# Kernel tuning notes

Hardware: AMD Instinct MI355X
Metric: run time of the kernel (lower is better)

Reference implementation:

```python
import jax, jax.numpy as jnp
import numpy as np

B, S, E, H = 2, 2048, 768, 8
D = E // H  # 96
SCALING = D ** (-0.5)


def setup_inputs() -> dict:
    key = jax.random.key(0)
    ks = jax.random.split(key, 7)
    sd = E ** -0.5
    return {
        "x": jax.random.normal(ks[0], (B, S, E), jnp.float32),
        "Wq": jax.random.normal(ks[1], (E, E), jnp.float32) * sd,
        "bq": jax.random.normal(ks[2], (E,), jnp.float32) * 0.02,
        "Wk": jax.random.normal(ks[3], (E, E), jnp.float32) * sd,
        "bk": jax.random.normal(ks[4], (E,), jnp.float32) * 0.02,
        "Wo": jax.random.normal(ks[5], (E, E), jnp.float32) * sd,
        "bo": jax.random.normal(ks[6], (E,), jnp.float32) * 0.02,
    }


def _split_heads(t):
    # [B, S, E] -> [B, H, S, D]
    return t.reshape(B, S, H, D).transpose(0, 2, 1, 3)


def reference(x, Wq, bq, Wk, bk, Wo, bo):
    q = _split_heads(x @ Wq + bq)
    k = _split_heads(x @ Wk + bk)
    # NOTE: faithful to source bug — values use the KEY projection
    v = _split_heads(x @ Wk + bk)
    energies = jnp.einsum("bhqd,bhkd->bhqk", q, k)  # [B,H,S,S]
    # NOTE: faithful to source — scaling applied AFTER softmax
    attn = jax.nn.softmax(energies, axis=-1) * SCALING
    out = jnp.einsum("bhqk,bhkd->bhqd", attn, v)
    out = out.transpose(0, 2, 1, 3).reshape(B, S, E)
    return out @ Wo + bo
```

## Files before the change

kernel.cpp:

```cpp
#include <hip/hip_runtime.h>
#include <hip/hip_bf16.h>
#include <math.h>
#include <stdint.h>

#define B_DIM 2
#define S_DIM 2048
#define E_DIM 768
#define H_DIM 8
#define D_DIM 96
#define M_DIM (B_DIM*S_DIM)
#define SCALE_F 0.10206207261596575f

typedef _Float16 f16x8 __attribute__((ext_vector_type(8)));
typedef float    f32x4  __attribute__((ext_vector_type(4)));
typedef float    f32x16 __attribute__((ext_vector_type(16)));

#define MFMA16H(a,b,c) __builtin_amdgcn_mfma_f32_16x16x32_f16(a,b,c,0,0,0)
#define MFMA32H(a,b,c) __builtin_amdgcn_mfma_f32_32x32x16_f16(a,b,c,0,0,0)

__device__ inline unsigned short f2h(float f) {
    return __builtin_bit_cast(unsigned short, (_Float16)f);
}

__device__ inline void gload16(const void* g, void* l) {
    auto gp = reinterpret_cast<const __attribute__((address_space(1))) uint32_t*>(
        reinterpret_cast<uintptr_t>(g));
    auto lp = reinterpret_cast<__attribute__((address_space(3))) uint32_t*>(
        reinterpret_cast<uintptr_t>(l));
    __builtin_amdgcn_global_load_lds(gp, lp, 16, 0, 0);
}

__global__ __launch_bounds__(256) void prep_kernel(
    const float* __restrict__ X,
    const float* __restrict__ W0, const float* __restrict__ W1,
    const float* __restrict__ W2,
    unsigned short* __restrict__ Xf,
    unsigned short* __restrict__ T0, unsigned short* __restrict__ T1,
    unsigned short* __restrict__ T2)
{
    const int tid = threadIdx.x;
    if (blockIdx.x < 3072) {
        int i = (blockIdx.x * 256 + tid) * 4;
        float4 v = *(const float4*)(X + i);
        ushort4 h;
        h.x = f2h(v.x); h.y = f2h(v.y); h.z = f2h(v.z); h.w = f2h(v.w);
        *(ushort4*)(Xf + i) = h;
        return;
    }
    int idx = blockIdx.x - 3072;
    int z = idx / 144, rem = idx % 144;
    const float* W; unsigned short* T;
    if (z == 0)      { W = W0; T = T0; }
    else if (z == 1) { W = W1; T = T1; }
    else             { W = W2; T = T2; }
    int k0 = (rem / 12) << 6, n0 = (rem % 12) << 6;

    __shared__ float tile[64][65];
    const int r = tid >> 4, c4 = (tid & 15) << 2;
    #pragma unroll
    for (int i = 0; i < 4; ++i) {
        float4 v = *(const float4*)(W + (size_t)(k0 + r + i*16)*E_DIM + n0 + c4);
        tile[r + i*16][c4+0] = v.x; tile[r + i*16][c4+1] = v.y;
        tile[r + i*16][c4+2] = v.z; tile[r + i*16][c4+3] = v.w;
    }
    __syncthreads();
    #pragma unroll
    for (int i = 0; i < 4; ++i) {
        int n = r + i*16;
        ushort4 h;
        h.x = f2h(tile[c4+0][n]); h.y = f2h(tile[c4+1][n]);
        h.z = f2h(tile[c4+2][n]); h.w = f2h(tile[c4+3][n]);
        *(ushort4*)(T + (size_t)(n0 + n)*E_DIM + k0 + c4) = h;
    }
}

__global__ __launch_bounds__(256) void gemm_qk_kernel(
    const unsigned short* __restrict__ A, const unsigned short* __restrict__ Bt,
    const float* __restrict__ bq, const float* __restrict__ bk,
    unsigned short* __restrict__ Qf, unsigned short* __restrict__ Kf)
{
    __shared__ unsigned short sA[128*32];
    __shared__ unsigned short sB[64*32];

    const int tid  = threadIdx.x;
    const int lane = tid & 63;
    const int w    = tid >> 6;
    const int qn   = lane & 15, quad = lane >> 4;
    const int wm   = w & 1, wn = w >> 1;
    const int row0 = blockIdx.y << 7;
    const int col0 = blockIdx.x << 6;

    const int sr = tid >> 2;
    const int sk = (tid & 3) << 3;

    const unsigned short* gA = A  + (size_t)(row0 + sr)*E_DIM + sk;
    const unsigned short* gB = Bt + (size_t)(col0 + sr)*E_DIM + sk;

    f32x4 acc[4][2];
    #pragma unroll
    for (int mt = 0; mt < 4; ++mt)
        #pragma unroll
        for (int nt = 0; nt < 2; ++nt)
            { acc[mt][nt][0]=0.f; acc[mt][nt][1]=0.f; acc[mt][nt][2]=0.f; acc[mt][nt][3]=0.f; }

    for (int k0 = 0; k0 < E_DIM; k0 += 32) {
        __syncthreads();
        gload16(gA + k0,            sA + tid*8);
        gload16(gA + 64*E_DIM + k0, sA + 2048 + tid*8);
        gload16(gB + k0,            sB + tid*8);
        __syncthreads();

        f16x8 af[4], bf[2];
        #pragma unroll
        for (int mt = 0; mt < 4; ++mt)
            af[mt] = *(const f16x8*)&sA[(wm*64 + mt*16 + qn)*32 + quad*8];
        #pragma unroll
        for (int nt = 0; nt < 2; ++nt)
            bf[nt] = *(const f16x8*)&sB[(wn*32 + nt*16 + qn)*32 + quad*8];
        #pragma unroll
        for (int mt = 0; mt < 4; ++mt)
            #pragma unroll
            for (int nt = 0; nt < 2; ++nt)
                acc[mt][nt] = MFMA16H(af[mt], bf[nt], acc[mt][nt]);
    }

    #pragma unroll
    for (int nt = 0; nt < 2; ++nt) {
        int n = col0 + wn*32 + nt*16 + qn;
        bool isQ = n < E_DIM;
        float bias = isQ ? bq[n] : bk[n - E_DIM];
        unsigned short* op = isQ ? Qf : Kf;
        int nc = isQ ? n : n - E_DIM;
        #pragma unroll
        for (int mt = 0; mt < 4; ++mt)
            #pragma unroll
            for (int r = 0; r < 4; ++r) {
                int m = row0 + wm*64 + mt*16 + quad*4 + r;
                op[(size_t)m*E_DIM + nc] = f2h(acc[mt][nt][r] + bias);
            }
    }
}

__global__ __launch_bounds__(256) void attn_mfma_kernel(
    const unsigned short* __restrict__ Qf, const unsigned short* __restrict__ Kf,
    unsigned short* __restrict__ O0, unsigned short* __restrict__ O1,
    float2* __restrict__ ml)
{
    __shared__ unsigned short sKh[64][104];
    __shared__ unsigned short sKt[96][72];
    __shared__ unsigned short sPs[128][72];

    const int tid  = threadIdx.x;
    const int w    = tid >> 6;
    const int lane = tid & 63;
    const int col  = lane & 31;
    const int half = lane >> 5;
    const int b    = blockIdx.z >> 1;
    const int kh   = blockIdx.z & 1;
    const int h    = blockIdx.y;
    const int q0   = blockIdx.x << 7;
    const int key0 = kh << 10;

    f16x8 qf[6];
    {
        const size_t ro = ((size_t)(b*S_DIM + q0 + w*32 + col))*E_DIM
                          + h*D_DIM + half*8;
        #pragma unroll
        for (int kc = 0; kc < 6; ++kc)
            qf[kc] = *(const f16x8*)(Qf + ro + kc*16);
    }

    f32x16 o[3];
    #pragma unroll
    for (int nt = 0; nt < 3; ++nt)
        #pragma unroll
        for (int r = 0; r < 16; ++r) o[nt][r] = 0.f;
    float m_i = -INFINITY, l_i = 0.f;

    const bool stager = tid < 128;
    const int st = tid & 127;
    const int sp = st >> 2;
    const int dq = st & 3;

    uint4 r0[3], r1[3];
    if (stager) {
        const size_t g0 = ((size_t)(b*S_DIM + key0 + 2*sp))*E_DIM + h*D_DIM + dq*24;
        #pragma unroll
        for (int i = 0; i < 3; ++i) {
            r0[i] = *(const uint4*)(Kf + g0 + 8*i);
            r1[i] = *(const uint4*)(Kf + g0 + E_DIM + 8*i);
        }
    }

    for (int kt = 0; kt < 16; ++kt) {
        __syncthreads();
        if (stager) {
            #pragma unroll
            for (int i = 0; i < 3; ++i) {
                *(uint4*)&sKh[2*sp  ][dq*24 + 8*i] = r0[i];
                *(uint4*)&sKh[2*sp+1][dq*24 + 8*i] = r1[i];
            }
            const unsigned short* p0 = (const unsigned short*)r0;
            const unsigned short* p1 = (const unsigned short*)r1;
            #pragma unroll
            for (int c = 0; c < 24; ++c) {
                unsigned int pk = (unsigned int)p0[c] | ((unsigned int)p1[c] << 16);
                *(unsigned int*)&sKt[dq*24 + c][2*sp] = pk;
            }
        }
        __syncthreads();

        if (stager && kt + 1 < 16) {
            const size_t g0 = ((size_t)(b*S_DIM + key0 + (kt+1)*64 + 2*sp))*E_DIM
                              + h*D_DIM + dq*24;
            #pragma unroll
            for (int i = 0; i < 3; ++i) {
                r0[i] = *(const uint4*)(Kf + g0 + 8*i);
                r1[i] = *(const uint4*)(Kf + g0 + E_DIM + 8*i);
            }
        }

        f32x16 s[2];
        #pragma unroll
        for (int mt = 0; mt < 2; ++mt) {
            f32x16 acc;
            #pragma unroll
            for (int r = 0; r < 16; ++r) acc[r] = 0.f;
            #pragma unroll
            for (int kc = 0; kc < 6; ++kc) {
                f16x8 ah = *(const f16x8*)&sKh[mt*32 + col][kc*16 + half*8];
                acc = MFMA32H(ah, qf[kc], acc);
            }
            s[mt] = acc;
        }

        float mx = s[0][0];
        #pragma unroll
        for (int mt = 0; mt < 2; ++mt)
            #pragma unroll
            for (int r = 0; r < 16; ++r) mx = fmaxf(mx, s[mt][r]);
        mx = fmaxf(mx, __shfl_xor(mx, 32));

        float m_new = fmaxf(m_i, mx);
        float alpha = __expf(m_i - m_new);
        m_i = m_new;

        float psum = 0.f;
        #pragma unroll
        for (int mt = 0; mt < 2; ++mt)
            #pragma unroll
            for (int g = 0; g < 4; ++g) {
                float e0 = __expf(s[mt][4*g+0] - m_new);
                float e1 = __expf(s[mt][4*g+1] - m_new);
                float e2 = __expf(s[mt][4*g+2] - m_new);
                float e3 = __expf(s[mt][4*g+3] - m_new);
                psum += e0 + e1 + e2 + e3;
                ushort4 pk;
                pk.x = f2h(e0); pk.y = f2h(e1); pk.z = f2h(e2); pk.w = f2h(e3);
                *(ushort4*)&sPs[w*32 + col][mt*32 + 8*g + 4*half] = pk;
            }
        psum += __shfl_xor(psum, 32);
        l_i = l_i * alpha + psum;

        #pragma unroll
        for (int nt = 0; nt < 3; ++nt)
            #pragma unroll
            for (int r = 0; r < 16; ++r) o[nt][r] *= alpha;

        #pragma unroll
        for (int kc = 0; kc < 4; ++kc) {
            f16x8 pb = *(const f16x8*)&sPs[w*32 + col][kc*16 + half*8];
            #pragma unroll
            for (int nt = 0; nt < 3; ++nt) {
                f16x8 va = *(const f16x8*)&sKt[nt*32 + col][kc*16 + half*8];
                o[nt] = MFMA32H(va, pb, o[nt]);
            }
        }
    }

    unsigned short* Ob = (kh ? O1 : O0)
        + ((size_t)(b*S_DIM + q0 + w*32 + col))*E_DIM + h*D_DIM;
    #pragma unroll
    for (int nt = 0; nt < 3; ++nt)
        #pragma unroll
        for (int rg = 0; rg < 4; ++rg) {
            ushort4 pk;
            pk.x = f2h(o[nt][4*rg+0]); pk.y = f2h(o[nt][4*rg+1]);
            pk.z = f2h(o[nt][4*rg+2]); pk.w = f2h(o[nt][4*rg+3]);
            *(ushort4*)(Ob + nt*32 + 8*rg + 4*half) = pk;
        }
    if (lane < 32) {
        int q = q0 + w*32 + lane;
        ml[((size_t)(kh*B_DIM + b)*H_DIM + h)*S_DIM + q] = make_float2(m_i, l_i);
    }
}

__device__ inline float2 mkscale(const float2* __restrict__ ml, int m, int h) {
    int b = m >> 11, q = m & (S_DIM - 1);
    float2 e0 = ml[((size_t)b*H_DIM + h)*S_DIM + q];
    float2 e1 = ml[((size_t)(B_DIM + b)*H_DIM + h)*S_DIM + q];
    float mm = fmaxf(e0.x, e1.x);
    float w0 = __expf(e0.x - mm), w1 = __expf(e1.x - mm);
    float inv = SCALE_F / (e0.y*w0 + e1.y*w1);
    return make_float2(w0*inv, w1*inv);
}

__global__ __launch_bounds__(256) void gemm_out_kernel(
    const unsigned short* __restrict__ O0, const unsigned short* __restrict__ O1,
    const float2* __restrict__ ml, const unsigned short* __restrict__ Bt,
    const float* __restrict__ bo, float* __restrict__ out)
{
    __shared__ unsigned short sA[64*32];
    __shared__ unsigned short sB[64*32];

    const int tid  = threadIdx.x;
    const int lane = tid & 63;
    const int w    = tid >> 6;
    const int qn   = lane & 15, quad = lane >> 4;
    const int wm   = w & 1, wn = w >> 1;
    const int row0 = blockIdx.y << 6;
    const int col0 = blockIdx.x << 6;

    const int ar = tid >> 2;
    const int ak = (tid & 3) << 3;

    const size_t r0o = (size_t)(row0 + ar)*E_DIM;
    const unsigned short* gB = Bt + (size_t)(col0 + ar)*E_DIM + ak;

    f32x4 acc[2][2];
    #pragma unroll
    for (int mt = 0; mt < 2; ++mt)
        #pragma unroll
        for (int nt = 0; nt < 2; ++nt)
            { acc[mt][nt][0]=0.f; acc[mt][nt][1]=0.f; acc[mt][nt][2]=0.f; acc[mt][nt][3]=0.f; }

    f16x8 u0 = *(const f16x8*)(O0 + r0o + ak);
    f16x8 v0 = *(const f16x8*)(O1 + r0o + ak);
    float2 s0 = mkscale(ml, row0 + ar, 0);

    for (int k0 = 0; k0 < E_DIM; k0 += 32) {
        __syncthreads();
        {
            f16x8 c0 = u0 * (_Float16)s0.x + v0 * (_Float16)s0.y;
            *(f16x8*)&sA[ar*32 + ak] = c0;
        }
        gload16(gB + k0, sB + tid*8);
        __syncthreads();

        if (k0 + 32 < E_DIM) {
            int kn = k0 + 32;
            u0 = *(const f16x8*)(O0 + r0o + kn + ak);
            v0 = *(const f16x8*)(O1 + r0o + kn + ak);
            s0 = mkscale(ml, row0 + ar, kn / D_DIM);
        }

        f16x8 af[2], bf[2];
        #pragma unroll
        for (int mt = 0; mt < 2; ++mt)
            af[mt] = *(const f16x8*)&sA[(wm*32 + mt*16 + qn)*32 + quad*8];
        #pragma unroll
        for (int nt = 0; nt < 2; ++nt)
            bf[nt] = *(const f16x8*)&sB[(wn*32 + nt*16 + qn)*32 + quad*8];
        #pragma unroll
        for (int mt = 0; mt < 2; ++mt)
            #pragma unroll
            for (int nt = 0; nt < 2; ++nt)
                acc[mt][nt] = MFMA16H(af[mt], bf[nt], acc[mt][nt]);
    }

    #pragma unroll
    for (int nt = 0; nt < 2; ++nt) {
        int n = col0 + wn*32 + nt*16 + qn;
        float bias = bo[n];
        #pragma unroll
        for (int mt = 0; mt < 2; ++mt)
            #pragma unroll
            for (int r = 0; r < 4; ++r) {
                int m = row0 + wm*32 + mt*16 + quad*4 + r;
                out[(size_t)m*E_DIM + n] = acc[mt][nt][r] + bias;
            }
    }
}

extern "C" void kernel_launch(void* const* d_in, const int* in_sizes, int n_in,
                              void* d_out, int out_size, void* d_ws, size_t ws_size,
                              hipStream_t stream)
{
    const float* x  = (const float*)d_in[0];
    const float* Wq = (const float*)d_in[1];
    const float* bq = (const float*)d_in[2];
    const float* Wk = (const float*)d_in[3];
    const float* bk = (const float*)d_in[4];
    const float* Wo = (const float*)d_in[5];
    const float* bo = (const float*)d_in[6];
    float* out = (float*)d_out;

    const size_t NE = (size_t)M_DIM * E_DIM;
    const size_t WE = (size_t)E_DIM * E_DIM;
    unsigned short* xf    = (unsigned short*)d_ws;
    unsigned short* WqkT  = xf + NE;
    unsigned short* WoT   = WqkT + 2*WE;
    unsigned short* Qf    = WoT + WE;
    unsigned short* Kf    = Qf + NE;
    unsigned short* Oh1   = Kf + NE;
    float2*         mlbuf = (float2*)(Oh1 + NE);
    unsigned short* Oh0   = xf;

    dim3 blk(256);
    hipLaunchKernelGGL(prep_kernel, dim3(3504), blk, 0, stream,
                       x, Wq, Wk, Wo, xf, WqkT, WqkT + WE, WoT);

    hipLaunchKernelGGL(gemm_qk_kernel, dim3(24,32), blk, 0, stream,
                       xf, WqkT, bq, bk, Qf, Kf);

    hipLaunchKernelGGL(attn_mfma_kernel, dim3(S_DIM/128, H_DIM, B_DIM*2), blk, 0,
                       stream, Qf, Kf, Oh0, Oh1, mlbuf);

    hipLaunchKernelGGL(gemm_out_kernel, dim3(12,64), blk, 0, stream,
                       Oh0, Oh1, mlbuf, WoT, bo, out);
}
```

Baseline: 168.6 us.

## Compute softmax row sums via MFMA with ones, widen QK GEMM k-step

The attention kernel drops the scalar row-sum reduction and cross-lane shuffle. It instead computes the softmax denominator with an extra MFMA that multiplies a ones vector by the P tile, so the sum is accumulated on the matrix cores and rescaled by alpha through one element. The row max uses three-input max trees, and fp16 packing uses the packed round-toward-zero convert. The QK projection GEMM loads 64-wide K chunks per sync, halving the number of barriers, at the cost of doubled LDS use; the extra MFMA per kc step adds matrix work and accumulator registers.

```diff
diff --git a/kernel.cpp b/kernel.cpp
--- a/kernel.cpp
+++ b/kernel.cpp
@@ -11,6 +11,7 @@
 #define M_DIM (B_DIM*S_DIM)
 #define SCALE_F 0.10206207261596575f
 
+typedef _Float16 f16x2 __attribute__((ext_vector_type(2)));
 typedef _Float16 f16x8 __attribute__((ext_vector_type(8)));
 typedef float    f32x4  __attribute__((ext_vector_type(4)));
 typedef float    f32x16 __attribute__((ext_vector_type(16)));
@@ -20,6 +21,12 @@
 
 __device__ inline unsigned short f2h(float f) {
     return __builtin_bit_cast(unsigned short, (_Float16)f);
+}
+__device__ inline unsigned int pk2(float a, float b) {
+    return __builtin_bit_cast(unsigned int, __builtin_amdgcn_cvt_pkrtz(a, b));
+}
+__device__ inline float max3f(float a, float b, float c) {
+    return fmaxf(fmaxf(a, b), c);
 }
 
 __device__ inline void gload16(const void* g, void* l) {
@@ -79,8 +86,8 @@
     const float* __restrict__ bq, const float* __restrict__ bk,
     unsigned short* __restrict__ Qf, unsigned short* __restrict__ Kf)
 {
-    __shared__ unsigned short sA[128*32];
-    __shared__ unsigned short sB[64*32];
+    __shared__ unsigned short sA[2*128*32];
+    __shared__ unsigned short sB[2*64*32];
 
     const int tid  = threadIdx.x;
     const int lane = tid & 63;
@@ -90,11 +97,11 @@
     const int row0 = blockIdx.y << 7;
     const int col0 = blockIdx.x << 6;
 
-    const int sr = tid >> 2;
-    const int sk = (tid & 3) << 3;
-
-    const unsigned short* gA = A  + (size_t)(row0 + sr)*E_DIM + sk;
-    const unsigned short* gB = Bt + (size_t)(col0 + sr)*E_DIM + sk;
+    const int ar = tid >> 2;
+    const int ak = (tid & 3) << 3;
+
+    const unsigned short* gA = A  + (size_t)(row0 + ar)*E_DIM + ak;
+    const unsigned short* gB = Bt + (size_t)(col0 + ar)*E_DIM + ak;
 
     f32x4 acc[4][2];
     #pragma unroll
@@ -103,25 +110,31 @@
         for (int nt = 0; nt < 2; ++nt)
             { acc[mt][nt][0]=0.f; acc[mt][nt][1]=0.f; acc[mt][nt][2]=0.f; acc[mt][nt][3]=0.f; }
 
-    for (int k0 = 0; k0 < E_DIM; k0 += 32) {
-        __syncthreads();
-        gload16(gA + k0,            sA + tid*8);
-        gload16(gA + 64*E_DIM + k0, sA + 2048 + tid*8);
-        gload16(gB + k0,            sB + tid*8);
-        __syncthreads();
-
-        f16x8 af[4], bf[2];
-        #pragma unroll
-        for (int mt = 0; mt < 4; ++mt)
-            af[mt] = *(const f16x8*)&sA[(wm*64 + mt*16 + qn)*32 + quad*8];
-        #pragma unroll
-        for (int nt = 0; nt < 2; ++nt)
-            bf[nt] = *(const f16x8*)&sB[(wn*32 + nt*16 + qn)*32 + quad*8];
-        #pragma unroll
-        for (int mt = 0; mt < 4; ++mt)
+    for (int k0 = 0; k0 < E_DIM; k0 += 64) {
+        __syncthreads();
+        gload16(gA + k0,                 sA + tid*8);
+        gload16(gA + 64*E_DIM + k0,      sA + 2048 + tid*8);
+        gload16(gA + k0 + 32,            sA + 4096 + tid*8);
+        gload16(gA + 64*E_DIM + k0 + 32, sA + 6144 + tid*8);
+        gload16(gB + k0,                 sB + tid*8);
+        gload16(gB + k0 + 32,            sB + 2048 + tid*8);
+        __syncthreads();
+
+        #pragma unroll
+        for (int kk = 0; kk < 2; ++kk) {
+            f16x8 af[4], bf[2];
+            #pragma unroll
+            for (int mt = 0; mt < 4; ++mt)
+                af[mt] = *(const f16x8*)&sA[kk*4096 + (wm*64 + mt*16 + qn)*32 + quad*8];
             #pragma unroll
             for (int nt = 0; nt < 2; ++nt)
-                acc[mt][nt] = MFMA16H(af[mt], bf[nt], acc[mt][nt]);
+                bf[nt] = *(const f16x8*)&sB[kk*2048 + (wn*32 + nt*16 + qn)*32 + quad*8];
+            #pragma unroll
+            for (int mt = 0; mt < 4; ++mt)
+                #pragma unroll
+                for (int nt = 0; nt < 2; ++nt)
+                    acc[mt][nt] = MFMA16H(af[mt], bf[nt], acc[mt][nt]);
+        }
     }
 
     #pragma unroll
@@ -170,12 +183,18 @@
             qf[kc] = *(const f16x8*)(Qf + ro + kc*16);
     }
 
-    f32x16 o[3];
+    f16x8 vones;
+    #pragma unroll
+    for (int i = 0; i < 8; ++i) vones[i] = (_Float16)1.0f;
+
+    f32x16 o[3], o4;
     #pragma unroll
     for (int nt = 0; nt < 3; ++nt)
         #pragma unroll
         for (int r = 0; r < 16; ++r) o[nt][r] = 0.f;
-    float m_i = -INFINITY, l_i = 0.f;
+    #pragma unroll
+    for (int r = 0; r < 16; ++r) o4[r] = 0.f;
+    float m_i = -INFINITY;
 
     const bool stager = tid < 128;
     const int st = tid & 127;
@@ -234,18 +253,30 @@
             s[mt] = acc;
         }
 
-        float mx = s[0][0];
-        #pragma unroll
-        for (int mt = 0; mt < 2; ++mt)
-            #pragma unroll
-            for (int r = 0; r < 16; ++r) mx = fmaxf(mx, s[mt][r]);
+        float mx;
+        {
+            float t0 = max3f(s[0][0], s[0][1], s[0][2]);
+            float t1 = max3f(s[0][3], s[0][4], s[0][5]);
+            float t2 = max3f(s[0][6], s[0][7], s[0][8]);
+            float t3 = max3f(s[0][9], s[0][10], s[0][11]);
+            float t4 = max3f(s[0][12], s[0][13], s[0][14]);
+            float u0 = max3f(s[1][0], s[1][1], s[1][2]);
+            float u1 = max3f(s[1][3], s[1][4], s[1][5]);
+            float u2 = max3f(s[1][6], s[1][7], s[1][8]);
+            float u3 = max3f(s[1][9], s[1][10], s[1][11]);
+            float u4 = max3f(s[1][12], s[1][13], s[1][14]);
+            float v0 = max3f(t0, t1, t2);
+            float v1 = max3f(t3, t4, s[0][15]);
+            float v2 = max3f(u0, u1, u2);
+            float v3 = max3f(u3, u4, s[1][15]);
+            mx = max3f(max3f(v0, v1, v2), v3, -INFINITY);
+        }
         mx = fmaxf(mx, __shfl_xor(mx, 32));
 
         float m_new = fmaxf(m_i, mx);
         float alpha = __expf(m_i - m_new);
         m_i = m_new;
 
-        float psum = 0.f;
         #pragma unroll
         for (int mt = 0; mt < 2; ++mt)
             #pragma unroll
@@ -254,18 +285,17 @@
                 float e1 = __expf(s[mt][4*g+1] - m_new);
                 float e2 = __expf(s[mt][4*g+2] - m_new);
                 float e3 = __expf(s[mt][4*g+3] - m_new);
-                psum += e0 + e1 + e2 + e3;
-                ushort4 pk;
-                pk.x = f2h(e0); pk.y = f2h(e1); pk.z = f2h(e2); pk.w = f2h(e3);
-                *(ushort4*)&sPs[w*32 + col][mt*32 + 8*g + 4*half] = pk;
-            }
-        psum += __shfl_xor(psum, 32);
-        l_i = l_i * alpha + psum;
+                uint2 pk;
+                pk.x = pk2(e0, e1);
+                pk.y = pk2(e2, e3);
+                *(uint2*)&sPs[w*32 + col][mt*32 + 8*g + 4*half] = pk;
+            }
 
         #pragma unroll
         for (int nt = 0; nt < 3; ++nt)
             #pragma unroll
             for (int r = 0; r < 16; ++r) o[nt][r] *= alpha;
+        o4[0] *= alpha;
 
         #pragma unroll
         for (int kc = 0; kc < 4; ++kc) {
@@ -275,6 +305,7 @@
                 f16x8 va = *(const f16x8*)&sKt[nt*32 + col][kc*16 + half*8];
                 o[nt] = MFMA32H(va, pb, o[nt]);
             }
+            o4 = MFMA32H(vones, pb, o4);
         }
     }
 
@@ -284,14 +315,14 @@
     for (int nt = 0; nt < 3; ++nt)
         #pragma unroll
         for (int rg = 0; rg < 4; ++rg) {
-            ushort4 pk;
-            pk.x = f2h(o[nt][4*rg+0]); pk.y = f2h(o[nt][4*rg+1]);
-            pk.z = f2h(o[nt][4*rg+2]); pk.w = f2h(o[nt][4*rg+3]);
-            *(ushort4*)(Ob + nt*32 + 8*rg + 4*half) = pk;
+            uint2 pk;
+            pk.x = pk2(o[nt][4*rg+0], o[nt][4*rg+1]);
+            pk.y = pk2(o[nt][4*rg+2], o[nt][4*rg+3]);
+            *(uint2*)(Ob + nt*32 + 8*rg + 4*half) = pk;
         }
     if (lane < 32) {
         int q = q0 + w*32 + lane;
-        ml[((size_t)(kh*B_DIM + b)*H_DIM + h)*S_DIM + q] = make_float2(m_i, l_i);
+        ml[((size_t)(kh*B_DIM + b)*H_DIM + h)*S_DIM + q] = make_float2(m_i, o4[0]);
     }
 }
 
```

After: 167.7 us. Within noise of the previous version (-0.5%).

## Split attention keys three ways and double the QK GEMM k-step

Applied to the files above, without the earlier changes.

The attention kernel now splits the key range into three chunks (11, 11 and 10 tiles) instead of two, launching 384 blocks rather than 256 so more CUs are busy, and writes a third partial output buffer. The output GEMM merges three partials with a three-way log-sum-exp rescale and only recomputes the scales at head boundaries. The QK GEMM loads 64 k-columns per barrier pair instead of 32, halving synchronisation. Costs are an extra partial buffer to write and read, more workspace, and more shared memory in the QK GEMM.

```diff
diff --git a/kernel.cpp b/kernel.cpp
--- a/kernel.cpp
+++ b/kernel.cpp
@@ -79,8 +79,8 @@
     const float* __restrict__ bq, const float* __restrict__ bk,
     unsigned short* __restrict__ Qf, unsigned short* __restrict__ Kf)
 {
-    __shared__ unsigned short sA[128*32];
-    __shared__ unsigned short sB[64*32];
+    __shared__ unsigned short sA[2*128*32];
+    __shared__ unsigned short sB[2*64*32];
 
     const int tid  = threadIdx.x;
     const int lane = tid & 63;
@@ -90,11 +90,11 @@
     const int row0 = blockIdx.y << 7;
     const int col0 = blockIdx.x << 6;
 
-    const int sr = tid >> 2;
-    const int sk = (tid & 3) << 3;
-
-    const unsigned short* gA = A  + (size_t)(row0 + sr)*E_DIM + sk;
-    const unsigned short* gB = Bt + (size_t)(col0 + sr)*E_DIM + sk;
+    const int ar = tid >> 2;
+    const int ak = (tid & 3) << 3;
+
+    const unsigned short* gA = A  + (size_t)(row0 + ar)*E_DIM + ak;
+    const unsigned short* gB = Bt + (size_t)(col0 + ar)*E_DIM + ak;
 
     f32x4 acc[4][2];
     #pragma unroll
@@ -103,25 +103,31 @@
         for (int nt = 0; nt < 2; ++nt)
             { acc[mt][nt][0]=0.f; acc[mt][nt][1]=0.f; acc[mt][nt][2]=0.f; acc[mt][nt][3]=0.f; }
 
-    for (int k0 = 0; k0 < E_DIM; k0 += 32) {
-        __syncthreads();
-        gload16(gA + k0,            sA + tid*8);
-        gload16(gA + 64*E_DIM + k0, sA + 2048 + tid*8);
-        gload16(gB + k0,            sB + tid*8);
-        __syncthreads();
-
-        f16x8 af[4], bf[2];
-        #pragma unroll
-        for (int mt = 0; mt < 4; ++mt)
-            af[mt] = *(const f16x8*)&sA[(wm*64 + mt*16 + qn)*32 + quad*8];
-        #pragma unroll
-        for (int nt = 0; nt < 2; ++nt)
-            bf[nt] = *(const f16x8*)&sB[(wn*32 + nt*16 + qn)*32 + quad*8];
-        #pragma unroll
-        for (int mt = 0; mt < 4; ++mt)
+    for (int k0 = 0; k0 < E_DIM; k0 += 64) {
+        __syncthreads();
+        gload16(gA + k0,                 sA + tid*8);
+        gload16(gA + 64*E_DIM + k0,      sA + 2048 + tid*8);
+        gload16(gA + k0 + 32,            sA + 4096 + tid*8);
+        gload16(gA + 64*E_DIM + k0 + 32, sA + 6144 + tid*8);
+        gload16(gB + k0,                 sB + tid*8);
+        gload16(gB + k0 + 32,            sB + 2048 + tid*8);
+        __syncthreads();
+
+        #pragma unroll
+        for (int kk = 0; kk < 2; ++kk) {
+            f16x8 af[4], bf[2];
+            #pragma unroll
+            for (int mt = 0; mt < 4; ++mt)
+                af[mt] = *(const f16x8*)&sA[kk*4096 + (wm*64 + mt*16 + qn)*32 + quad*8];
             #pragma unroll
             for (int nt = 0; nt < 2; ++nt)
-                acc[mt][nt] = MFMA16H(af[mt], bf[nt], acc[mt][nt]);
+                bf[nt] = *(const f16x8*)&sB[kk*2048 + (wn*32 + nt*16 + qn)*32 + quad*8];
+            #pragma unroll
+            for (int mt = 0; mt < 4; ++mt)
+                #pragma unroll
+                for (int nt = 0; nt < 2; ++nt)
+                    acc[mt][nt] = MFMA16H(af[mt], bf[nt], acc[mt][nt]);
+        }
     }
 
     #pragma unroll
@@ -144,7 +150,7 @@
 __global__ __launch_bounds__(256) void attn_mfma_kernel(
     const unsigned short* __restrict__ Qf, const unsigned short* __restrict__ Kf,
     unsigned short* __restrict__ O0, unsigned short* __restrict__ O1,
-    float2* __restrict__ ml)
+    unsigned short* __restrict__ O2, float2* __restrict__ ml)
 {
     __shared__ unsigned short sKh[64][104];
     __shared__ unsigned short sKt[96][72];
@@ -155,11 +161,13 @@
     const int lane = tid & 63;
     const int col  = lane & 31;
     const int half = lane >> 5;
-    const int b    = blockIdx.z >> 1;
-    const int kh   = blockIdx.z & 1;
+    const int z    = blockIdx.z;
+    const int b    = z / 3;
+    const int kv   = z % 3;
     const int h    = blockIdx.y;
     const int q0   = blockIdx.x << 7;
-    const int key0 = kh << 10;
+    const int key0 = kv * 704;
+    const int ktiles = (kv < 2) ? 11 : 10;
 
     f16x8 qf[6];
     {
@@ -192,7 +200,7 @@
         }
     }
 
-    for (int kt = 0; kt < 16; ++kt) {
+    for (int kt = 0; kt < ktiles; ++kt) {
         __syncthreads();
         if (stager) {
             #pragma unroll
@@ -210,7 +218,7 @@
         }
         __syncthreads();
 
-        if (stager && kt + 1 < 16) {
+        if (stager && kt + 1 < ktiles) {
             const size_t g0 = ((size_t)(b*S_DIM + key0 + (kt+1)*64 + 2*sp))*E_DIM
                               + h*D_DIM + dq*24;
             #pragma unroll
@@ -278,7 +286,7 @@
         }
     }
 
-    unsigned short* Ob = (kh ? O1 : O0)
+    unsigned short* Ob = (kv == 0 ? O0 : kv == 1 ? O1 : O2)
         + ((size_t)(b*S_DIM + q0 + w*32 + col))*E_DIM + h*D_DIM;
     #pragma unroll
     for (int nt = 0; nt < 3; ++nt)
@@ -291,24 +299,28 @@
         }
     if (lane < 32) {
         int q = q0 + w*32 + lane;
-        ml[((size_t)(kh*B_DIM + b)*H_DIM + h)*S_DIM + q] = make_float2(m_i, l_i);
-    }
-}
-
-__device__ inline float2 mkscale(const float2* __restrict__ ml, int m, int h) {
+        ml[((size_t)(kv*B_DIM + b)*H_DIM + h)*S_DIM + q] = make_float2(m_i, l_i);
+    }
+}
+
+struct Sc3 { float x, y, z; };
+__device__ inline Sc3 mkscale3(const float2* __restrict__ ml, int m, int h) {
     int b = m >> 11, q = m & (S_DIM - 1);
-    float2 e0 = ml[((size_t)b*H_DIM + h)*S_DIM + q];
-    float2 e1 = ml[((size_t)(B_DIM + b)*H_DIM + h)*S_DIM + q];
-    float mm = fmaxf(e0.x, e1.x);
-    float w0 = __expf(e0.x - mm), w1 = __expf(e1.x - mm);
-    float inv = SCALE_F / (e0.y*w0 + e1.y*w1);
-    return make_float2(w0*inv, w1*inv);
+    float2 e0 = ml[((size_t)(0*B_DIM + b)*H_DIM + h)*S_DIM + q];
+    float2 e1 = ml[((size_t)(1*B_DIM + b)*H_DIM + h)*S_DIM + q];
+    float2 e2 = ml[((size_t)(2*B_DIM + b)*H_DIM + h)*S_DIM + q];
+    float mm = fmaxf(fmaxf(e0.x, e1.x), e2.x);
+    float w0 = __expf(e0.x - mm), w1 = __expf(e1.x - mm), w2 = __expf(e2.x - mm);
+    float inv = SCALE_F / (e0.y*w0 + e1.y*w1 + e2.y*w2);
+    Sc3 s; s.x = w0*inv; s.y = w1*inv; s.z = w2*inv;
+    return s;
 }
 
 __global__ __launch_bounds__(256) void gemm_out_kernel(
     const unsigned short* __restrict__ O0, const unsigned short* __restrict__ O1,
-    const float2* __restrict__ ml, const unsigned short* __restrict__ Bt,
-    const float* __restrict__ bo, float* __restrict__ out)
+    const unsigned short* __restrict__ O2, const float2* __restrict__ ml,
+    const unsigned short* __restrict__ Bt, const float* __restrict__ bo,
+    float* __restrict__ out)
 {
     __shared__ unsigned short sA[64*32];
     __shared__ unsigned short sB[64*32];
@@ -336,12 +348,14 @@
 
     f16x8 u0 = *(const f16x8*)(O0 + r0o + ak);
     f16x8 v0 = *(const f16x8*)(O1 + r0o + ak);
-    float2 s0 = mkscale(ml, row0 + ar, 0);
+    f16x8 t0 = *(const f16x8*)(O2 + r0o + ak);
+    Sc3 s3 = mkscale3(ml, row0 + ar, 0);
+    _Float16 hx = (_Float16)s3.x, hy = (_Float16)s3.y, hz = (_Float16)s3.z;
 
     for (int k0 = 0; k0 < E_DIM; k0 += 32) {
         __syncthreads();
         {
-            f16x8 c0 = u0 * (_Float16)s0.x + v0 * (_Float16)s0.y;
+            f16x8 c0 = u0 * hx + v0 * hy + t0 * hz;
             *(f16x8*)&sA[ar*32 + ak] = c0;
         }
         gload16(gB + k0, sB + tid*8);
@@ -351,7 +365,11 @@
             int kn = k0 + 32;
             u0 = *(const f16x8*)(O0 + r0o + kn + ak);
             v0 = *(const f16x8*)(O1 + r0o + kn + ak);
-            s0 = mkscale(ml, row0 + ar, kn / D_DIM);
+            t0 = *(const f16x8*)(O2 + r0o + kn + ak);
+            if ((kn % D_DIM) == 0) {
+                s3 = mkscale3(ml, row0 + ar, kn / D_DIM);
+                hx = (_Float16)s3.x; hy = (_Float16)s3.y; hz = (_Float16)s3.z;
+            }
         }
 
         f16x8 af[2], bf[2];
@@ -403,7 +421,8 @@
     unsigned short* Qf    = WoT + WE;
     unsigned short* Kf    = Qf + NE;
     unsigned short* Oh1   = Kf + NE;
-    float2*         mlbuf = (float2*)(Oh1 + NE);
+    unsigned short* Oh2   = Oh1 + NE;
+    float2*         mlbuf = (float2*)(Oh2 + NE);
     unsigned short* Oh0   = xf;
 
     dim3 blk(256);
@@ -413,9 +432,9 @@
     hipLaunchKernelGGL(gemm_qk_kernel, dim3(24,32), blk, 0, stream,
                        xf, WqkT, bq, bk, Qf, Kf);
 
-    hipLaunchKernelGGL(attn_mfma_kernel, dim3(S_DIM/128, H_DIM, B_DIM*2), blk, 0,
-                       stream, Qf, Kf, Oh0, Oh1, mlbuf);
+    hipLaunchKernelGGL(attn_mfma_kernel, dim3(S_DIM/128, H_DIM, B_DIM*3), blk, 0,
+                       stream, Qf, Kf, Oh0, Oh1, Oh2, mlbuf);
 
     hipLaunchKernelGGL(gemm_out_kernel, dim3(12,64), blk, 0, stream,
-                       Oh0, Oh1, mlbuf, WoT, bo, out);
-}
+                       Oh0, Oh1, Oh2, mlbuf, WoT, bo, out);
+}
```

Measured after the change: 178.3 us. +5.8%, slower.

## Double-buffer attention K tiles, widen QK GEMM k-step, cache output scales

Applied to the files above, without the earlier changes.

The attention kernel now keeps two shared K/K-transpose buffers that alternate per tile. This removes the leading barrier of each iteration, so staging the next tile can overlap compute on the current one. The QK projection GEMM now loads 64 columns of k per barrier pair instead of 32, halving the number of barriers, but it doubles shared memory use. The output GEMM recomputes the per-head merge scales only when crossing a head boundary rather than every k-step. The attention change depends on a single barrier per iteration staying race-free, since the sPs buffer reuse is unchanged.

```diff
diff --git a/kernel.cpp b/kernel.cpp
--- a/kernel.cpp
+++ b/kernel.cpp
@@ -79,8 +79,8 @@
     const float* __restrict__ bq, const float* __restrict__ bk,
     unsigned short* __restrict__ Qf, unsigned short* __restrict__ Kf)
 {
-    __shared__ unsigned short sA[128*32];
-    __shared__ unsigned short sB[64*32];
+    __shared__ unsigned short sA[2*128*32];
+    __shared__ unsigned short sB[2*64*32];
 
     const int tid  = threadIdx.x;
     const int lane = tid & 63;
@@ -90,11 +90,11 @@
     const int row0 = blockIdx.y << 7;
     const int col0 = blockIdx.x << 6;
 
-    const int sr = tid >> 2;
-    const int sk = (tid & 3) << 3;
-
-    const unsigned short* gA = A  + (size_t)(row0 + sr)*E_DIM + sk;
-    const unsigned short* gB = Bt + (size_t)(col0 + sr)*E_DIM + sk;
+    const int ar = tid >> 2;
+    const int ak = (tid & 3) << 3;
+
+    const unsigned short* gA = A  + (size_t)(row0 + ar)*E_DIM + ak;
+    const unsigned short* gB = Bt + (size_t)(col0 + ar)*E_DIM + ak;
 
     f32x4 acc[4][2];
     #pragma unroll
@@ -103,25 +103,31 @@
         for (int nt = 0; nt < 2; ++nt)
             { acc[mt][nt][0]=0.f; acc[mt][nt][1]=0.f; acc[mt][nt][2]=0.f; acc[mt][nt][3]=0.f; }
 
-    for (int k0 = 0; k0 < E_DIM; k0 += 32) {
+    for (int k0 = 0; k0 < E_DIM; k0 += 64) {
         __syncthreads();
-        gload16(gA + k0,            sA + tid*8);
-        gload16(gA + 64*E_DIM + k0, sA + 2048 + tid*8);
-        gload16(gB + k0,            sB + tid*8);
+        gload16(gA + k0,                 sA + tid*8);
+        gload16(gA + 64*E_DIM + k0,      sA + 2048 + tid*8);
+        gload16(gA + k0 + 32,            sA + 4096 + tid*8);
+        gload16(gA + 64*E_DIM + k0 + 32, sA + 6144 + tid*8);
+        gload16(gB + k0,                 sB + tid*8);
+        gload16(gB + k0 + 32,            sB + 2048 + tid*8);
         __syncthreads();
 
-        f16x8 af[4], bf[2];
-        #pragma unroll
-        for (int mt = 0; mt < 4; ++mt)
-            af[mt] = *(const f16x8*)&sA[(wm*64 + mt*16 + qn)*32 + quad*8];
-        #pragma unroll
-        for (int nt = 0; nt < 2; ++nt)
-            bf[nt] = *(const f16x8*)&sB[(wn*32 + nt*16 + qn)*32 + quad*8];
-        #pragma unroll
-        for (int mt = 0; mt < 4; ++mt)
+        #pragma unroll
+        for (int kk = 0; kk < 2; ++kk) {
+            f16x8 af[4], bf[2];
+            #pragma unroll
+            for (int mt = 0; mt < 4; ++mt)
+                af[mt] = *(const f16x8*)&sA[kk*4096 + (wm*64 + mt*16 + qn)*32 + quad*8];
             #pragma unroll
             for (int nt = 0; nt < 2; ++nt)
-                acc[mt][nt] = MFMA16H(af[mt], bf[nt], acc[mt][nt]);
+                bf[nt] = *(const f16x8*)&sB[kk*2048 + (wn*32 + nt*16 + qn)*32 + quad*8];
+            #pragma unroll
+            for (int mt = 0; mt < 4; ++mt)
+                #pragma unroll
+                for (int nt = 0; nt < 2; ++nt)
+                    acc[mt][nt] = MFMA16H(af[mt], bf[nt], acc[mt][nt]);
+        }
     }
 
     #pragma unroll
@@ -146,8 +152,8 @@
     unsigned short* __restrict__ O0, unsigned short* __restrict__ O1,
     float2* __restrict__ ml)
 {
-    __shared__ unsigned short sKh[64][104];
-    __shared__ unsigned short sKt[96][72];
+    __shared__ unsigned short sKh[2][64][104];
+    __shared__ unsigned short sKt[2][96][72];
     __shared__ unsigned short sPs[128][72];
 
     const int tid  = threadIdx.x;
@@ -193,19 +199,19 @@
     }
 
     for (int kt = 0; kt < 16; ++kt) {
-        __syncthreads();
+        const int p = kt & 1;
         if (stager) {
             #pragma unroll
             for (int i = 0; i < 3; ++i) {
-                *(uint4*)&sKh[2*sp  ][dq*24 + 8*i] = r0[i];
-                *(uint4*)&sKh[2*sp+1][dq*24 + 8*i] = r1[i];
+                *(uint4*)&sKh[p][2*sp  ][dq*24 + 8*i] = r0[i];
+                *(uint4*)&sKh[p][2*sp+1][dq*24 + 8*i] = r1[i];
             }
             const unsigned short* p0 = (const unsigned short*)r0;
             const unsigned short* p1 = (const unsigned short*)r1;
             #pragma unroll
             for (int c = 0; c < 24; ++c) {
                 unsigned int pk = (unsigned int)p0[c] | ((unsigned int)p1[c] << 16);
-                *(unsigned int*)&sKt[dq*24 + c][2*sp] = pk;
+                *(unsigned int*)&sKt[p][dq*24 + c][2*sp] = pk;
             }
         }
         __syncthreads();
@@ -228,7 +234,7 @@
             for (int r = 0; r < 16; ++r) acc[r] = 0.f;
             #pragma unroll
             for (int kc = 0; kc < 6; ++kc) {
-                f16x8 ah = *(const f16x8*)&sKh[mt*32 + col][kc*16 + half*8];
+                f16x8 ah = *(const f16x8*)&sKh[p][mt*32 + col][kc*16 + half*8];
                 acc = MFMA32H(ah, qf[kc], acc);
             }
             s[mt] = acc;
@@ -272,7 +278,7 @@
             f16x8 pb = *(const f16x8*)&sPs[w*32 + col][kc*16 + half*8];
             #pragma unroll
             for (int nt = 0; nt < 3; ++nt) {
-                f16x8 va = *(const f16x8*)&sKt[nt*32 + col][kc*16 + half*8];
+                f16x8 va = *(const f16x8*)&sKt[p][nt*32 + col][kc*16 + half*8];
                 o[nt] = MFMA32H(va, pb, o[nt]);
             }
         }
@@ -337,11 +343,12 @@
     f16x8 u0 = *(const f16x8*)(O0 + r0o + ak);
     f16x8 v0 = *(const f16x8*)(O1 + r0o + ak);
     float2 s0 = mkscale(ml, row0 + ar, 0);
+    _Float16 hx = (_Float16)s0.x, hy = (_Float16)s0.y;
 
     for (int k0 = 0; k0 < E_DIM; k0 += 32) {
         __syncthreads();
         {
-            f16x8 c0 = u0 * (_Float16)s0.x + v0 * (_Float16)s0.y;
+            f16x8 c0 = u0 * hx + v0 * hy;
             *(f16x8*)&sA[ar*32 + ak] = c0;
         }
         gload16(gB + k0, sB + tid*8);
@@ -351,7 +358,10 @@
             int kn = k0 + 32;
             u0 = *(const f16x8*)(O0 + r0o + kn + ak);
             v0 = *(const f16x8*)(O1 + r0o + kn + ak);
-            s0 = mkscale(ml, row0 + ar, kn / D_DIM);
+            if ((kn % D_DIM) == 0) {
+                s0 = mkscale(ml, row0 + ar, kn / D_DIM);
+                hx = (_Float16)s0.x; hy = (_Float16)s0.y;
+            }
         }
 
         f16x8 af[2], bf[2];
```

Result: faster. 163.8 us (-2.8%).
